# Performance work log

Hardware: AMD Instinct MI355X
Metric: run time of the kernel (lower is better)

The kernel has to match this reference:

```python
import jax, jax.numpy as jnp
import numpy as np

# TT factorized linear: weight of shape (768, 768) factorized as 6-mode tensor
# modes = [12,8,8,8,8,12]; first 3 modes are input factorization (12*8*8=768),
# last 3 are output factorization (8*8*12=768). TT ranks r = [1,5,5,5,5,5,1].
MODES = [12, 8, 8, 8, 8, 12]
RANK = 5
IN_MODES = MODES[:3]   # 12,8,8
OUT_MODES = MODES[3:]  # 8,8,12
HID = 768


def tt_ranks():
    return [1] + [RANK] * (len(MODES) - 1) + [1]


def setup_inputs() -> dict:
    key = jax.random.key(0)
    ks = jax.random.split(key, len(MODES) + 2)
    hidden_states = jax.random.normal(ks[0], (8, 512, HID), dtype=jnp.float32)
    r = tt_ranks()
    cores = {}
    for i, m in enumerate(MODES):
        # core_i shape: (r_i, m_i, r_{i+1})
        std = 1.0 / np.sqrt(m * r[i])
        cores[f"core{i}"] = jax.random.normal(ks[i + 1], (r[i], m, r[i + 1]), dtype=jnp.float32) * std
    bias = jnp.zeros((HID,), dtype=jnp.float32)
    return {"hidden_states": hidden_states, "bias": bias, **cores}


def tt_linear(x, cores, bias):
    # x: (..., 768) -> reshape to (..., 12, 8, 8)
    lead = x.shape[:-1]
    B = int(np.prod(lead))
    t = x.reshape(B, IN_MODES[0], IN_MODES[1], IN_MODES[2])
    # contract input modes with first 3 cores, threading the TT rank
    # start: carry rank r0=1
    t = t[..., None]  # (B, m0, m1, m2, r0=1) after moving? simpler: explicit einsums
    t = x.reshape(B, 12, 8, 8)
    # core0: (1,12,r1) -> (B, 8, 8, r1)
    t = jnp.einsum('bijk,aiv->bjkv', t, cores[0])
    # core1: (r1,8,r2) -> (B, 8, r2)
    t = jnp.einsum('bjkv,vjw->bkw', t, cores[1])
    # core2: (r2,8,r3) -> (B, r3)
    t = jnp.einsum('bkw,wkx->bx', t, cores[2])
    # expand output modes with last 3 cores
    # core3: (r3,8,r4) -> (B, 8, r4)
    t = jnp.einsum('bx,xpy->bpy', t, cores[3])
    # core4: (r4,8,r5) -> (B, 8, 8, r5)
    t = jnp.einsum('bpy,yqz->bpqz', t, cores[4])
    # core5: (r5,12,1) -> (B, 8, 8, 12)
    t = jnp.einsum('bpqz,zra->bpqr', t, cores[5])
    out = t.reshape(*lead, HID) + bias
    return out


def reference(hidden_states, bias, core0, core1, core2, core3, core4, core5):
    cores = [core0, core1, core2, core3, core4, core5]
    out = tt_linear(hidden_states, cores, bias)
    activated = jax.nn.gelu(out, approximate=False)
    return hidden_states + activated
```

## Files before the change

### kernel.cpp

```cpp
#include <hip/hip_runtime.h>
#include <math.h>

#define HID 768
#define RANK 5


__device__ __forceinline__ float gelu_f(float v) {
    return 0.5f * v * (1.0f + erff(v * 0.70710678118654752f));
}

__global__ __launch_bounds__(1024) void tt_fused(
    const float* __restrict__ x, const float* __restrict__ bias,
    const float* __restrict__ c0, const float* __restrict__ c1,
    const float* __restrict__ c2, const float* __restrict__ c3,
    const float* __restrict__ c4, const float* __restrict__ c5,
    float* __restrict__ out, int Btot) {
    __shared__ __align__(16) float sW1[RANK * HID];
    __shared__ __align__(16) float sW2[RANK * HID];
    __shared__ __align__(16) float sB[HID];

    const int tid = threadIdx.x;
    const int lane = tid & 63;
    const int wave = tid >> 6;
    const int row = blockIdx.x * (blockDim.x >> 6) + wave;
    const bool active = row < Btot;

    float4 xv0, xv1, xv2;
    if (active) {
        const float4* xr = reinterpret_cast<const float4*>(x + (size_t)row * HID);
        xv0 = xr[lane];
        xv1 = xr[lane + 64];
        xv2 = xr[lane + 128];
    }

    if (tid < HID) {
        const int h = tid;
        {
            const int i = h >> 6, j = (h >> 3) & 7, k = h & 7;
            float acc[RANK] = {0.f, 0.f, 0.f, 0.f, 0.f};
#pragma unroll
            for (int v = 0; v < RANK; ++v) {
                const float a = c0[i * RANK + v];
#pragma unroll
                for (int w = 0; w < RANK; ++w) {
                    const float e = a * c1[(v * 8 + j) * RANK + w];
                    const float* c2p = &c2[(w * 8 + k) * RANK];
#pragma unroll
                    for (int xx = 0; xx < RANK; ++xx) acc[xx] += e * c2p[xx];
                }
            }
#pragma unroll
            for (int xx = 0; xx < RANK; ++xx) sW1[xx * HID + h] = acc[xx];
        }
        {
            const int p = h / 96, q = (h / 12) & 7, r = h % 12;
            float acc[RANK] = {0.f, 0.f, 0.f, 0.f, 0.f};
#pragma unroll
            for (int y = 0; y < RANK; ++y) {
#pragma unroll
                for (int z = 0; z < RANK; ++z) {
                    const float e = c4[(y * 8 + q) * RANK + z] * c5[z * 12 + r];
#pragma unroll
                    for (int xx = 0; xx < RANK; ++xx)
                        acc[xx] += c3[(xx * 8 + p) * RANK + y] * e;
                }
            }
#pragma unroll
            for (int xx = 0; xx < RANK; ++xx) sW2[xx * HID + h] = acc[xx];
        }
    } else if (tid - HID < HID / 4) {
        const int t = tid - HID;
        reinterpret_cast<float4*>(sB)[t] = reinterpret_cast<const float4*>(bias)[t];
    }

    __syncthreads();

    if (!active) return;

    float acc[RANK];
    const float4* w1v = reinterpret_cast<const float4*>(sW1);
#pragma unroll
    for (int j = 0; j < RANK; ++j) {
        float4 a = w1v[j * 192 + lane];
        float4 b = w1v[j * 192 + lane + 64];
        float4 c = w1v[j * 192 + lane + 128];
        acc[j] = xv0.x * a.x + xv0.y * a.y + xv0.z * a.z + xv0.w * a.w
               + xv1.x * b.x + xv1.y * b.y + xv1.z * b.z + xv1.w * b.w
               + xv2.x * c.x + xv2.y * c.y + xv2.z * c.z + xv2.w * c.w;
    }
#pragma unroll
    for (int off = 32; off >= 1; off >>= 1) {
#pragma unroll
        for (int j = 0; j < RANK; ++j) acc[j] += __shfl_xor(acc[j], off, 64);
    }

    const float4* w2v = reinterpret_cast<const float4*>(sW2);
    const float4* bv  = reinterpret_cast<const float4*>(sB);
    float4* outr = reinterpret_cast<float4*>(out + (size_t)row * HID);
#pragma unroll
    for (int t = 0; t < 3; ++t) {
        const int idx = lane + 64 * t;
        float4 o = bv[idx];
#pragma unroll
        for (int j = 0; j < RANK; ++j) {
            float4 w = w2v[j * 192 + idx];
            o.x += acc[j] * w.x;
            o.y += acc[j] * w.y;
            o.z += acc[j] * w.z;
            o.w += acc[j] * w.w;
        }
        const float4 xv = (t == 0) ? xv0 : (t == 1) ? xv1 : xv2;
        o.x = xv.x + gelu_f(o.x);
        o.y = xv.y + gelu_f(o.y);
        o.z = xv.z + gelu_f(o.z);
        o.w = xv.w + gelu_f(o.w);
        outr[idx] = o;
    }
}

extern "C" void kernel_launch(void* const* d_in, const int* in_sizes, int n_in,
                              void* d_out, int out_size, void* d_ws, size_t ws_size,
                              hipStream_t stream) {
    const float* hs   = (const float*)d_in[0];
    const float* bias = (const float*)d_in[1];
    const float* c0   = (const float*)d_in[2];
    const float* c1   = (const float*)d_in[3];
    const float* c2   = (const float*)d_in[4];
    const float* c3   = (const float*)d_in[5];
    const float* c4   = (const float*)d_in[6];
    const float* c5   = (const float*)d_in[7];
    float* out = (float*)d_out;

    const int Btot = in_sizes[0] / HID;

    const int wavesPerBlock = 16;
    const int grid = (Btot + wavesPerBlock - 1) / wavesPerBlock;
    tt_fused<<<grid, wavesPerBlock * 64, 0, stream>>>(
        hs, bias, c0, c1, c2, c3, c4, c5, out, Btot);
}
```

Baseline: 14.86 us.

## Factor TT weight reconstruction through shared partial contractions and use fast GELU

Precomputes the c1·c2 and c4·c5 partial contractions once per block into shared memory, so each thread's reconstruction of the rank-5 input and output projections needs far fewer multiply-adds and global loads. Also replaces the erf-based GELU with a tanh-style approximation built from a fast exp and a hardware reciprocal. This adds a second block barrier and a little shared memory, and the GELU change introduces small numerical differences from exact GELU.

```diff
diff --git a/kernel.cpp b/kernel.cpp
--- a/kernel.cpp
+++ b/kernel.cpp
@@ -6,7 +6,9 @@
 
 
 __device__ __forceinline__ float gelu_f(float v) {
-    return 0.5f * v * (1.0f + erff(v * 0.70710678118654752f));
+    const float z = v * (1.5957691216f + 0.0713548162726f * v * v);
+    const float e = __expf(z);
+    return v * e * __builtin_amdgcn_rcpf(1.0f + e);
 }
 
 __global__ __launch_bounds__(1024) void tt_fused(
@@ -18,11 +20,13 @@
     __shared__ __align__(16) float sW1[RANK * HID];
     __shared__ __align__(16) float sW2[RANK * HID];
     __shared__ __align__(16) float sB[HID];
+    __shared__ __align__(16) float sT1[5 * 8 * 8 * 5];
+    __shared__ __align__(16) float sU2[5 * 8 * 12];
 
     const int tid = threadIdx.x;
     const int lane = tid & 63;
     const int wave = tid >> 6;
-    const int row = blockIdx.x * (blockDim.x >> 6) + wave;
+    const int row = blockIdx.x * 16 + wave;
     const bool active = row < Btot;
 
     float4 xv0, xv1, xv2;
@@ -33,6 +37,32 @@
         xv2 = xr[lane + 128];
     }
 
+    if (tid < 320) {
+        const int v = tid >> 6, j = (tid >> 3) & 7, k = tid & 7;
+        float acc[RANK] = {0.f, 0.f, 0.f, 0.f, 0.f};
+#pragma unroll
+        for (int w = 0; w < RANK; ++w) {
+            const float e = c1[(v * 8 + j) * RANK + w];
+            const float* c2p = &c2[(w * 8 + k) * RANK];
+#pragma unroll
+            for (int xx = 0; xx < RANK; ++xx) acc[xx] += e * c2p[xx];
+        }
+#pragma unroll
+        for (int xx = 0; xx < RANK; ++xx) sT1[tid * RANK + xx] = acc[xx];
+    } else if (tid < 800) {
+        const int idx = tid - 320;
+        const int y = idx / 96, rem = idx % 96, q = rem / 12, r = rem % 12;
+        float acc = 0.f;
+#pragma unroll
+        for (int z = 0; z < RANK; ++z) acc += c4[(y * 8 + q) * RANK + z] * c5[z * 12 + r];
+        sU2[idx] = acc;
+    } else if (tid < 800 + HID / 4) {
+        const int t = tid - 800;
+        reinterpret_cast<float4*>(sB)[t] = reinterpret_cast<const float4*>(bias)[t];
+    }
+
+    __syncthreads();
+
     if (tid < HID) {
         const int h = tid;
         {
@@ -41,36 +71,26 @@
 #pragma unroll
             for (int v = 0; v < RANK; ++v) {
                 const float a = c0[i * RANK + v];
+                const float* tp = &sT1[((v * 8 + j) * 8 + k) * RANK];
 #pragma unroll
-                for (int w = 0; w < RANK; ++w) {
-                    const float e = a * c1[(v * 8 + j) * RANK + w];
-                    const float* c2p = &c2[(w * 8 + k) * RANK];
-#pragma unroll
-                    for (int xx = 0; xx < RANK; ++xx) acc[xx] += e * c2p[xx];
-                }
+                for (int xx = 0; xx < RANK; ++xx) acc[xx] += a * tp[xx];
             }
 #pragma unroll
             for (int xx = 0; xx < RANK; ++xx) sW1[xx * HID + h] = acc[xx];
         }
         {
             const int p = h / 96, q = (h / 12) & 7, r = h % 12;
-            float acc[RANK] = {0.f, 0.f, 0.f, 0.f, 0.f};
+            float u[RANK];
 #pragma unroll
-            for (int y = 0; y < RANK; ++y) {
+            for (int y = 0; y < RANK; ++y) u[y] = sU2[(y * 8 + q) * 12 + r];
 #pragma unroll
-                for (int z = 0; z < RANK; ++z) {
-                    const float e = c4[(y * 8 + q) * RANK + z] * c5[z * 12 + r];
+            for (int xx = 0; xx < RANK; ++xx) {
+                float acc = 0.f;
 #pragma unroll
-                    for (int xx = 0; xx < RANK; ++xx)
-                        acc[xx] += c3[(xx * 8 + p) * RANK + y] * e;
-                }
+                for (int y = 0; y < RANK; ++y) acc += c3[(xx * 8 + p) * RANK + y] * u[y];
+                sW2[xx * HID + h] = acc;
             }
-#pragma unroll
-            for (int xx = 0; xx < RANK; ++xx) sW2[xx * HID + h] = acc[xx];
         }
-    } else if (tid - HID < HID / 4) {
-        const int t = tid - HID;
-        reinterpret_cast<float4*>(sB)[t] = reinterpret_cast<const float4*>(bias)[t];
     }
 
     __syncthreads();
@@ -133,8 +153,7 @@
 
     const int Btot = in_sizes[0] / HID;
 
-    const int wavesPerBlock = 16;
-    const int grid = (Btot + wavesPerBlock - 1) / wavesPerBlock;
-    tt_fused<<<grid, wavesPerBlock * 64, 0, stream>>>(
+    const int grid = (Btot + 15) / 16;
+    tt_fused<<<grid, 1024, 0, stream>>>(
         hs, bias, c0, c1, c2, c3, c4, c5, out, Btot);
 }
```

New measurement: 13.09 us (median of 2 runs). 11.9% less time.
